# Optimization experiments

Measured on AMD Instinct MI355X. Metric: run time of the kernel, lower is better.

## Reference

```python
import jax, jax.numpy as jnp
import numpy as np

EPS = 1e-5


def _proj(x, W, b, g, beta):
    # Linear + LayerNorm over last axis (ProjectionFCNN with norm=True)
    h = jnp.einsum('bld,dh->blh', x, W) + b
    mu = jnp.mean(h, axis=-1, keepdims=True)
    var = jnp.var(h, axis=-1, keepdims=True)
    return (h - mu) * jax.lax.rsqrt(var + EPS) * g + beta


def setup_inputs() -> dict:
    key = jax.random.key(0)
    ks = jax.random.split(key, 8)
    B, L, DQ, DKV, H = 8, 2048, 512, 768, 512
    s = 0.02
    return {
        'query_sequence': jax.random.normal(ks[0], (B, L, DQ), jnp.float32),
        'key_value_sequence': jax.random.normal(ks[1], (B, L, DKV), jnp.float32),
        'Wq': jax.random.normal(ks[2], (DQ, H), jnp.float32) * s,
        'bq': jnp.zeros((H,), jnp.float32),
        'gq': jnp.ones((H,), jnp.float32),
        'betaq': jnp.zeros((H,), jnp.float32),
        'Wk': jax.random.normal(ks[3], (DKV, H), jnp.float32) * s,
        'bk': jnp.zeros((H,), jnp.float32),
        'gk': jnp.ones((H,), jnp.float32),
        'betak': jnp.zeros((H,), jnp.float32),
        'Wv': jax.random.normal(ks[4], (DKV, DQ), jnp.float32) * s,
        'bv': jnp.zeros((DQ,), jnp.float32),
        'gv': jnp.ones((DQ,), jnp.float32),
        'betav': jnp.zeros((DQ,), jnp.float32),
    }


def reference(query_sequence, key_value_sequence, Wq, bq, gq, betaq,
              Wk, bk, gk, betak, Wv, bv, gv, betav):
    query = _proj(query_sequence, Wq, bq, gq, betaq)          # [b, L, H]
    k = _proj(key_value_sequence, Wk, bk, gk, betak)          # [b, l, H]
    v = _proj(key_value_sequence, Wv, bv, gv, betav)          # [b, l, DQ]
    # attn_score: 'b l c, b L c -> b l L'; softmax over last (query) axis
    attn = jax.nn.softmax(jnp.einsum('blc,bLc->blL', k, query), axis=-1)
    out = jnp.einsum('blL,bLc->blc', attn, v)                 # [b, l, DQ]
    return out + query_sequence
```

## Files before the change

### kernel.cpp

```cpp
#include <hip/hip_runtime.h>

typedef _Float16 f16;
typedef _Float16 f16x4 __attribute__((ext_vector_type(4)));
typedef _Float16 f16x8 __attribute__((ext_vector_type(8)));
typedef float f32x4 __attribute__((ext_vector_type(4)));
typedef unsigned int u32;

#define NB   8
#define SEQ  2048
#define DQ_  512
#define DKV_ 768
#define HD_  512

__device__ __forceinline__ void gll16(const void* g, void* l) {
  __builtin_amdgcn_global_load_lds(
      (const __attribute__((address_space(1))) u32*)g,
      (__attribute__((address_space(3))) u32*)l, 16, 0, 0);
}

__global__ __launch_bounds__(256) void cast_transpose(const float* __restrict__ in,
                                                      f16* __restrict__ out,
                                                      int K, int N) {
  int i = blockIdx.x * 256 + threadIdx.x;
  if (i >= K * N) return;
  int n = i / K, k = i % K;
  out[i] = (f16)in[k * N + n];
}

__global__ __launch_bounds__(512) void proj_ln(
    const float* __restrict__ xq, const float* __restrict__ xkv,
    const f16* __restrict__ wqt, const f16* __restrict__ wkt, const f16* __restrict__ wvt,
    const float* __restrict__ bq, const float* __restrict__ gq, const float* __restrict__ beq,
    const float* __restrict__ bk, const float* __restrict__ gk, const float* __restrict__ bek,
    const float* __restrict__ bv, const float* __restrict__ gv, const float* __restrict__ bev,
    f16* __restrict__ outq, f16* __restrict__ outk, f16* __restrict__ outvt)
{
  __shared__ char smem[37888 + 4096 + 512];
  f16* Xs    = (f16*)smem;
  f16* Wts   = (f16*)(smem + 5120);
  f16* trans = (f16*)smem;
  float* red = (float*)(smem + 37888);
  float* mus = (float*)(smem + 37888 + 4096);
  float* rss = mus + 64;

  const int proj = blockIdx.x >> 8;
  const int tile = blockIdx.x & 255;
  const float* X; const f16* Wt; const float *bias, *gam, *bet; f16* out; int KD;
  if (proj == 0)      { X = xq;  Wt = wqt; bias = bq; gam = gq; bet = beq; out = outq;  KD = 512; }
  else if (proj == 1) { X = xkv; Wt = wkt; bias = bk; gam = gk; bet = bek; out = outk;  KD = 768; }
  else                { X = xkv; Wt = wvt; bias = bv; gam = gv; bet = bev; out = outvt; KD = 768; }

  const int row0 = tile * 64;
  const int tid = threadIdx.x;
  const int w = tid >> 6;
  const int lane = tid & 63;
  const int g = lane >> 4, tt = lane & 15;

  f32x4 acc[4][4] = {};

  const int nk = KD >> 5;
  for (int kt = 0; kt < nk; ++kt) {
    const int k0 = kt * 32;
    if (tid < 256) {
      int r = tid >> 2, c = tid & 3;
      const float* src = X + (size_t)(row0 + r) * KD + k0 + c * 8;
      float4 a = *(const float4*)src;
      float4 b = *(const float4*)(src + 4);
      f16x8 h;
      h[0] = (f16)a.x; h[1] = (f16)a.y; h[2] = (f16)a.z; h[3] = (f16)a.w;
      h[4] = (f16)b.x; h[5] = (f16)b.y; h[6] = (f16)b.z; h[7] = (f16)b.w;
      *(f16x8*)&Xs[r * 40 + c * 8] = h;
    }
    #pragma unroll
    for (int i = 0; i < 4; ++i) {
      int o = i * 8192 + tid * 16;
      int r = o >> 6;
      int c = (o >> 4) & 3;
      int cs = c ^ (r & 3);
      gll16(Wt + (size_t)r * KD + k0 + cs * 8, (char*)Wts + o);
    }
    __syncthreads();
    f16x8 af[4];
    #pragma unroll
    for (int m = 0; m < 4; ++m)
      af[m] = *(const f16x8*)&Xs[(m * 16 + tt) * 40 + g * 8];
    #pragma unroll
    for (int n = 0; n < 4; ++n) {
      int R = w * 64 + n * 16 + tt;
      int ch = g ^ (R & 3);
      f16x8 bf = *(const f16x8*)&Wts[R * 32 + ch * 8];
      #pragma unroll
      for (int m = 0; m < 4; ++m)
        acc[m][n] = __builtin_amdgcn_mfma_f32_16x16x32_f16(af[m], bf, acc[m][n], 0, 0, 0);
    }
    __syncthreads();
  }

  float bias4[4], gam4[4], bet4[4];
  #pragma unroll
  for (int n = 0; n < 4; ++n) {
    int c = w * 64 + n * 16 + tt;
    bias4[n] = bias[c]; gam4[n] = gam[c]; bet4[n] = bet[c];
  }
  float rsum[4][4], rsq[4][4];
  #pragma unroll
  for (int m = 0; m < 4; ++m)
    #pragma unroll
    for (int j = 0; j < 4; ++j) { rsum[m][j] = 0.f; rsq[m][j] = 0.f; }
  #pragma unroll
  for (int m = 0; m < 4; ++m)
    #pragma unroll
    for (int n = 0; n < 4; ++n)
      #pragma unroll
      for (int j = 0; j < 4; ++j) {
        float h = acc[m][n][j] + bias4[n];
        acc[m][n][j] = h;
        rsum[m][j] += h; rsq[m][j] += h * h;
      }
  #pragma unroll
  for (int mk = 1; mk < 16; mk <<= 1)
    #pragma unroll
    for (int m = 0; m < 4; ++m)
      #pragma unroll
      for (int j = 0; j < 4; ++j) {
        rsum[m][j] += __shfl_xor(rsum[m][j], mk);
        rsq[m][j]  += __shfl_xor(rsq[m][j], mk);
      }
  if (tt == 0) {
    #pragma unroll
    for (int m = 0; m < 4; ++m)
      #pragma unroll
      for (int j = 0; j < 4; ++j) {
        int r = m * 16 + g * 4 + j;
        red[(r * 8 + w) * 2 + 0] = rsum[m][j];
        red[(r * 8 + w) * 2 + 1] = rsq[m][j];
      }
  }
  __syncthreads();
  if (tid < 64) {
    float s = 0.f, sq = 0.f;
    #pragma unroll
    for (int w2 = 0; w2 < 8; ++w2) {
      s  += red[(tid * 8 + w2) * 2 + 0];
      sq += red[(tid * 8 + w2) * 2 + 1];
    }
    float mu = s * (1.f / 512.f);
    float var = sq * (1.f / 512.f) - mu * mu;
    mus[tid] = mu;
    rss[tid] = rsqrtf(var + 1e-5f);
  }
  __syncthreads();
  #pragma unroll
  for (int m = 0; m < 4; ++m)
    #pragma unroll
    for (int j = 0; j < 4; ++j) {
      int r = m * 16 + g * 4 + j;
      float mu = mus[r], rs = rss[r];
      #pragma unroll
      for (int n = 0; n < 4; ++n)
        acc[m][n][j] = (acc[m][n][j] - mu) * rs * gam4[n] + bet4[n];
    }

  if (proj != 2) {
    #pragma unroll
    for (int m = 0; m < 4; ++m)
      #pragma unroll
      for (int j = 0; j < 4; ++j) {
        int r = row0 + m * 16 + g * 4 + j;
        #pragma unroll
        for (int n = 0; n < 4; ++n)
          out[(size_t)r * 512 + w * 64 + n * 16 + tt] = (f16)acc[m][n][j];
      }
  } else {
    const int bch = row0 >> 11, l0 = row0 & 2047;
    __syncthreads();
    for (int half = 0; half < 2; ++half) {
      if ((w >> 2) == half) {
        #pragma unroll
        for (int m = 0; m < 4; ++m)
          #pragma unroll
          for (int n = 0; n < 4; ++n)
            #pragma unroll
            for (int j = 0; j < 4; ++j)
              trans[((w & 3) * 64 + n * 16 + tt) * 72 + (m * 16 + g * 4 + j)] =
                  (f16)acc[m][n][j];
      }
      __syncthreads();
      {
        int c = tid >> 1, ii = tid & 1;
        size_t gb = (size_t)bch * (512 * 2048) + (size_t)(half * 256 + c) * 2048
                    + l0 + ii * 32;
        #pragma unroll
        for (int q2 = 0; q2 < 4; ++q2)
          *(f16x8*)&out[gb + q2 * 8] = *(const f16x8*)&trans[c * 72 + ii * 32 + q2 * 8];
      }
      __syncthreads();
    }
  }
}

template <bool RESID, typename CT>
__global__ __launch_bounds__(256) void gemm_nt(
    const f16* __restrict__ A, const f16* __restrict__ Bt,
    CT* __restrict__ C, const float* __restrict__ resid,
    int K, int tilesM, int tilesN, int N,
    size_t sA, size_t sB, size_t sC)
{
  __shared__ f16 As[128 * 64];
  __shared__ f16 Bs[128 * 64];
  const int bpb = tilesM * tilesN;
  const int b = blockIdx.x / bpb;
  const int t = blockIdx.x % bpb;
  const int tm = t % tilesM, tn = t / tilesM;
  const f16* Ab  = A  + (size_t)b * sA + (size_t)tm * 128 * K;
  const f16* Btb = Bt + (size_t)b * sB + (size_t)tn * 128 * K;
  const int tid = threadIdx.x, w = tid >> 6, lane = tid & 63;
  const int wr = w >> 1, wc = w & 1;
  const int g = lane >> 4, tt = lane & 15;
  f32x4 acc[4][4] = {};
  for (int kt = 0; kt < K; kt += 64) {
    #pragma unroll
    for (int i = 0; i < 4; ++i) {
      int o = i * 4096 + tid * 16;
      int r = o >> 7;
      int c = (o >> 4) & 7;
      int cs = c ^ (r & 7);
      gll16(Ab  + (size_t)r * K + kt + cs * 8, (char*)As + o);
      gll16(Btb + (size_t)r * K + kt + cs * 8, (char*)Bs + o);
    }
    __syncthreads();
    #pragma unroll
    for (int kk = 0; kk < 2; ++kk) {
      f16x8 af[4], bf[4];
      #pragma unroll
      for (int m = 0; m < 4; ++m) {
        int R = wr * 64 + m * 16 + tt;
        int ch = (kk * 4 + g) ^ (R & 7);
        af[m] = *(const f16x8*)&As[R * 64 + ch * 8];
      }
      #pragma unroll
      for (int n = 0; n < 4; ++n) {
        int R = wc * 64 + n * 16 + tt;
        int ch = (kk * 4 + g) ^ (R & 7);
        bf[n] = *(const f16x8*)&Bs[R * 64 + ch * 8];
      }
      #pragma unroll
      for (int n = 0; n < 4; ++n)
        #pragma unroll
        for (int m = 0; m < 4; ++m)
          acc[m][n] = __builtin_amdgcn_mfma_f32_16x16x32_f16(af[m], bf[n], acc[m][n], 0, 0, 0);
    }
    __syncthreads();
  }
  const size_t Cb = (size_t)b * sC;
  #pragma unroll
  for (int m = 0; m < 4; ++m)
    #pragma unroll
    for (int j = 0; j < 4; ++j) {
      int r = tm * 128 + wr * 64 + m * 16 + g * 4 + j;
      #pragma unroll
      for (int n = 0; n < 4; ++n) {
        int c = tn * 128 + wc * 64 + n * 16 + tt;
        size_t idx = Cb + (size_t)r * N + c;
        float v = acc[m][n][j];
        if (RESID) v += resid[idx];
        C[idx] = (CT)v;
      }
    }
}

__global__ __launch_bounds__(256) void softmax_rows(f16* __restrict__ SP)
{
  __shared__ float sred[4];
  const size_t row = blockIdx.x;
  f16x8* Pr = (f16x8*)(SP + row * 2048);
  const int tid = threadIdx.x, w = tid >> 6, lane = tid & 63;
  f16x8 v = Pr[tid];
  float f[8];
  #pragma unroll
  for (int j = 0; j < 8; ++j) f[j] = (float)v[j];
  float mx = f[0];
  #pragma unroll
  for (int j = 1; j < 8; ++j) mx = fmaxf(mx, f[j]);
  #pragma unroll
  for (int mk = 1; mk < 64; mk <<= 1) mx = fmaxf(mx, __shfl_xor(mx, mk));
  if (lane == 0) sred[w] = mx;
  __syncthreads();
  mx = fmaxf(fmaxf(sred[0], sred[1]), fmaxf(sred[2], sred[3]));
  __syncthreads();
  float e[8], s = 0.f;
  #pragma unroll
  for (int j = 0; j < 8; ++j) { e[j] = __expf(f[j] - mx); s += e[j]; }
  #pragma unroll
  for (int mk = 1; mk < 64; mk <<= 1) s += __shfl_xor(s, mk);
  if (lane == 0) sred[w] = s;
  __syncthreads();
  s = sred[0] + sred[1] + sred[2] + sred[3];
  float inv = 1.f / s;
  f16x8 p;
  #pragma unroll
  for (int j = 0; j < 8; ++j) p[j] = (f16)(e[j] * inv);
  Pr[tid] = p;
}

extern "C" void kernel_launch(void* const* d_in, const int* in_sizes, int n_in,
                              void* d_out, int out_size, void* d_ws, size_t ws_size,
                              hipStream_t stream) {
  const float* qs   = (const float*)d_in[0];
  const float* kv   = (const float*)d_in[1];
  const float* Wq   = (const float*)d_in[2];
  const float* bq   = (const float*)d_in[3];
  const float* gq   = (const float*)d_in[4];
  const float* beq  = (const float*)d_in[5];
  const float* Wk   = (const float*)d_in[6];
  const float* bk   = (const float*)d_in[7];
  const float* gk   = (const float*)d_in[8];
  const float* bek  = (const float*)d_in[9];
  const float* Wv   = (const float*)d_in[10];
  const float* bv   = (const float*)d_in[11];
  const float* gv   = (const float*)d_in[12];
  const float* bev  = (const float*)d_in[13];
  float* out = (float*)d_out;

  char* ws = (char*)d_ws;
  f16* q16  = (f16*)(ws + 0);
  f16* k16  = (f16*)(ws + 16777216);
  f16* vt   = (f16*)(ws + 33554432);
  f16* Wqt  = (f16*)(ws + 50331648);
  f16* Wkt  = (f16*)(ws + 50855936);
  f16* Wvt  = (f16*)(ws + 51642368);
  f16* S    = (f16*)(ws + 52428800);

  cast_transpose<<<1024, 256, 0, stream>>>(Wq, Wqt, 512, 512);
  cast_transpose<<<1536, 256, 0, stream>>>(Wk, Wkt, 768, 512);
  cast_transpose<<<1536, 256, 0, stream>>>(Wv, Wvt, 768, 512);

  proj_ln<<<768, 512, 0, stream>>>(qs, kv, Wqt, Wkt, Wvt,
                                   bq, gq, beq, bk, gk, bek, bv, gv, bev,
                                   q16, k16, vt);

  gemm_nt<false, f16><<<2048, 256, 0, stream>>>(
      k16, q16, S, nullptr,
      512, 16, 16, 2048,
      (size_t)2048 * 512, (size_t)2048 * 512, (size_t)2048 * 2048);

  softmax_rows<<<16384, 256, 0, stream>>>(S);

  gemm_nt<true, float><<<512, 256, 0, stream>>>(
      S, vt, out, qs,
      2048, 16, 4, 512,
      (size_t)2048 * 2048, (size_t)512 * 2048, (size_t)2048 * 512);
}
```

Measured before the change: 356.5 us.

## Load projection weights directly to registers and remap GEMM blocks per XCD

The projection+LayerNorm kernel no longer stages the weight tile in LDS. Each wave now reads its B fragments straight from global memory (L2-cached, shared across blocks), while X is staged in 128-wide K strips to cut the number of barriers. The batched GEMM kernel remaps block IDs so that consecutive tiles from the same batch land on the same XCD, which is meant to improve L2 locality. The risk is that uncoalesced per-lane global weight loads raise latency and VGPR pressure. The remap also assumes the grid size is divisible by 8.

```diff
diff --git a/kernel.cpp b/kernel.cpp
--- a/kernel.cpp
+++ b/kernel.cpp
@@ -35,12 +35,11 @@
     const float* __restrict__ bv, const float* __restrict__ gv, const float* __restrict__ bev,
     f16* __restrict__ outq, f16* __restrict__ outk, f16* __restrict__ outvt)
 {
-  __shared__ char smem[37888 + 4096 + 512];
+  __shared__ char smem[36864 + 4096 + 512];
   f16* Xs    = (f16*)smem;
-  f16* Wts   = (f16*)(smem + 5120);
   f16* trans = (f16*)smem;
-  float* red = (float*)(smem + 37888);
-  float* mus = (float*)(smem + 37888 + 4096);
+  float* red = (float*)(smem + 36864);
+  float* mus = (float*)(smem + 36864 + 4096);
   float* rss = mus + 64;
 
   const int proj = blockIdx.x >> 8;
@@ -56,42 +55,47 @@
   const int lane = tid & 63;
   const int g = lane >> 4, tt = lane & 15;
 
+  const float* xrow = X + (size_t)(row0 + (tid >> 3)) * KD + (tid & 7) * 16;
+  const f16* wrow[4];
+  #pragma unroll
+  for (int n = 0; n < 4; ++n)
+    wrow[n] = Wt + (size_t)(w * 64 + n * 16 + tt) * KD + g * 8;
+
   f32x4 acc[4][4] = {};
 
-  const int nk = KD >> 5;
-  for (int kt = 0; kt < nk; ++kt) {
-    const int k0 = kt * 32;
-    if (tid < 256) {
-      int r = tid >> 2, c = tid & 3;
-      const float* src = X + (size_t)(row0 + r) * KD + k0 + c * 8;
-      float4 a = *(const float4*)src;
+  const int nstrip = KD >> 7;
+  for (int st = 0; st < nstrip; ++st) {
+    const int ks = st * 128;
+    {
+      const int r = tid >> 3, c0 = (tid & 7) * 16;
+      const float* src = xrow + ks;
+      float4 a = *(const float4*)(src);
       float4 b = *(const float4*)(src + 4);
-      f16x8 h;
-      h[0] = (f16)a.x; h[1] = (f16)a.y; h[2] = (f16)a.z; h[3] = (f16)a.w;
-      h[4] = (f16)b.x; h[5] = (f16)b.y; h[6] = (f16)b.z; h[7] = (f16)b.w;
-      *(f16x8*)&Xs[r * 40 + c * 8] = h;
-    }
-    #pragma unroll
-    for (int i = 0; i < 4; ++i) {
-      int o = i * 8192 + tid * 16;
-      int r = o >> 6;
-      int c = (o >> 4) & 3;
-      int cs = c ^ (r & 3);
-      gll16(Wt + (size_t)r * KD + k0 + cs * 8, (char*)Wts + o);
-    }
-    __syncthreads();
-    f16x8 af[4];
-    #pragma unroll
-    for (int m = 0; m < 4; ++m)
-      af[m] = *(const f16x8*)&Xs[(m * 16 + tt) * 40 + g * 8];
-    #pragma unroll
-    for (int n = 0; n < 4; ++n) {
-      int R = w * 64 + n * 16 + tt;
-      int ch = g ^ (R & 3);
-      f16x8 bf = *(const f16x8*)&Wts[R * 32 + ch * 8];
+      float4 c = *(const float4*)(src + 8);
+      float4 d = *(const float4*)(src + 12);
+      f16x8 h0, h1;
+      h0[0] = (f16)a.x; h0[1] = (f16)a.y; h0[2] = (f16)a.z; h0[3] = (f16)a.w;
+      h0[4] = (f16)b.x; h0[5] = (f16)b.y; h0[6] = (f16)b.z; h0[7] = (f16)b.w;
+      h1[0] = (f16)c.x; h1[1] = (f16)c.y; h1[2] = (f16)c.z; h1[3] = (f16)c.w;
+      h1[4] = (f16)d.x; h1[5] = (f16)d.y; h1[6] = (f16)d.z; h1[7] = (f16)d.w;
+      *(f16x8*)&Xs[r * 136 + c0]     = h0;
+      *(f16x8*)&Xs[r * 136 + c0 + 8] = h1;
+    }
+    __syncthreads();
+    #pragma unroll
+    for (int s = 0; s < 4; ++s) {
+      f16x8 af[4], bf[4];
+      #pragma unroll
+      for (int n = 0; n < 4; ++n)
+        bf[n] = *(const f16x8*)(wrow[n] + ks + s * 32);
       #pragma unroll
       for (int m = 0; m < 4; ++m)
-        acc[m][n] = __builtin_amdgcn_mfma_f32_16x16x32_f16(af[m], bf, acc[m][n], 0, 0, 0);
+        af[m] = *(const f16x8*)&Xs[(m * 16 + tt) * 136 + s * 32 + g * 8];
+      #pragma unroll
+      for (int n = 0; n < 4; ++n)
+        #pragma unroll
+        for (int m = 0; m < 4; ++m)
+          acc[m][n] = __builtin_amdgcn_mfma_f32_16x16x32_f16(af[m], bf[n], acc[m][n], 0, 0, 0);
     }
     __syncthreads();
   }
@@ -208,9 +212,12 @@
 {
   __shared__ f16 As[128 * 64];
   __shared__ f16 Bs[128 * 64];
+  const int nwg = gridDim.x;
+  const int orig = blockIdx.x;
+  const int bid = (orig & 7) * (nwg >> 3) + (orig >> 3);
   const int bpb = tilesM * tilesN;
-  const int b = blockIdx.x / bpb;
-  const int t = blockIdx.x % bpb;
+  const int b = bid / bpb;
+  const int t = bid % bpb;
   const int tm = t % tilesM, tn = t / tilesM;
   const f16* Ab  = A  + (size_t)b * sA + (size_t)tm * 128 * K;
   const f16* Btb = Bt + (size_t)b * sB + (size_t)tn * 128 * K;
```

New measurement: 354.3 us. About the same (-0.6%).
